# Optimization experiments

Measured on AMD Instinct MI355X. Metric: run time of the kernel, lower is better.

The kernel has to match this reference:

```python
import jax, jax.numpy as jnp
import numpy as np

B = 32768
N_INT = 32          # num_intruders
OWN_D = 3
INT_D = 7
ATTN_D = 128
HID = 256
OUT_D = 2
OBS_D = OWN_D + N_INT * INT_D  # 227
NEG_SLOPE = 0.2

def _lrelu(x):
    return jax.nn.leaky_relu(x, NEG_SLOPE)

def setup_inputs() -> dict:
    key = jax.random.key(0)
    ks = jax.random.split(key, 16)
    obs = jax.random.normal(ks[0], (B, OBS_D), dtype=jnp.float32)
    pad = jax.random.bernoulli(ks[1], 0.25, (B, N_INT))
    intr = obs[:, OWN_D:].reshape(B, N_INT, INT_D)
    intr = jnp.where(pad[:, :, None], 0.0, intr)
    obs = jnp.concatenate([obs[:, :OWN_D], intr.reshape(B, -1)], axis=1)
    def glorot(k, shape):
        fan_in, fan_out = shape[0], shape[-1]
        lim = jnp.sqrt(6.0 / (fan_in + fan_out))
        return jax.random.uniform(k, shape, jnp.float32, -lim, lim)
    return {
        "obs": obs,
        "own_W": glorot(ks[2], (OWN_D, ATTN_D)), "own_b": jnp.zeros((ATTN_D,), jnp.float32),
        "int_W": glorot(ks[3], (INT_D, ATTN_D)), "int_b": jnp.zeros((ATTN_D,), jnp.float32),
        "Wq": glorot(ks[4], (ATTN_D, ATTN_D)),
        "Wk": glorot(ks[5], (ATTN_D, ATTN_D)),
        "Wv": glorot(ks[6], (ATTN_D, ATTN_D)),
        "v_att": glorot(ks[7], (ATTN_D, 1))[:, 0],
        "proj_W": glorot(ks[8], (ATTN_D, ATTN_D)), "proj_b": jnp.zeros((ATTN_D,), jnp.float32),
        "h1_W": glorot(ks[9], (2 * ATTN_D, HID)), "h1_b": jnp.zeros((HID,), jnp.float32),
        "h2_W": glorot(ks[10], (HID, HID)), "h2_b": jnp.zeros((HID,), jnp.float32),
        "out_W": glorot(ks[11], (HID, OUT_D)), "out_b": jnp.zeros((OUT_D,), jnp.float32),
    }

def reference(obs, own_W, own_b, int_W, int_b, Wq, Wk, Wv, v_att,
              proj_W, proj_b, h1_W, h1_b, h2_W, h2_b, out_W, out_b):
    own = obs[:, :OWN_D]                                   # [B,3]
    intr = obs[:, OWN_D:OWN_D + N_INT * INT_D].reshape(-1, N_INT, INT_D)  # [B,N,7]
    own_e = _lrelu(own @ own_W + own_b)                    # [B,128]
    int_e = _lrelu(intr @ int_W + int_b)                   # [B,N,128]
    q = own_e @ Wq                                         # [B,128]
    k = int_e @ Wk                                         # [B,N,128]
    v = int_e @ Wv                                         # [B,N,128]
    energy = jnp.tanh(q[:, None, :] + k)                   # [B,N,128]
    scores = energy @ v_att                                # [B,N]
    is_padding = jnp.abs(intr).sum(axis=2) < 1e-6          # [B,N]
    scores = jnp.where(is_padding, -jnp.inf, scores)
    alpha = jax.nn.softmax(scores, axis=-1)
    alpha = jnp.nan_to_num(alpha, nan=0.0)
    ctx = jnp.einsum('bn,bnd->bd', alpha, v)               # [B,128]
    attn_vec = jnp.tanh(ctx @ proj_W + proj_b)             # [B,128]
    x = jnp.concatenate([own_e, attn_vec], axis=1)         # [B,256]
    x = _lrelu(x @ h1_W + h1_b)
    x = _lrelu(x @ h2_W + h2_b)
    return x @ out_W + out_b                               # [B,2]
```

## Files before the change

kernel.cpp:

```cpp
#include <hip/hip_runtime.h>
#include <hip/hip_bf16.h>
#include <math.h>

typedef _Float16 half2_t __attribute__((ext_vector_type(2)));
typedef _Float16 f16x8   __attribute__((ext_vector_type(8)));
typedef float    f32x4   __attribute__((ext_vector_type(4)));

constexpr int BATCH = 32768;
constexpr int NI   = 32;
constexpr int OWND = 3;
constexpr int INTD = 7;
constexpr int AD   = 128;
constexpr int HIDN = 256;
constexpr int OUTD = 2;
constexpr int OBSD = OWND + NI * INTD;
constexpr int IEPITCH = 68;
constexpr float C2L2E = 2.885390081777927f;

__device__ __forceinline__ half2_t u2h(unsigned u) { return __builtin_bit_cast(half2_t, u); }
__device__ __forceinline__ unsigned packf(float a, float b) {
    half2_t h = { (_Float16)a, (_Float16)b };
    return __builtin_bit_cast(unsigned, h);
}
__device__ __forceinline__ float lrelu(float x) { return fmaxf(x, 0.2f * x); }
__device__ __forceinline__ float exp2fast(float x) { return __builtin_amdgcn_exp2f(x); }
__device__ __forceinline__ float fast_tanh(float x) {
    float e = exp2fast(x * C2L2E);
    return 1.0f - 2.0f * __builtin_amdgcn_rcpf(e + 1.0f);
}

constexpr int UW_PWKQ = 0;
constexpr int UW_PWVF = 16384;
constexpr int UW_PPRF = 24576;
constexpr int UW_PIWF = 32768;
constexpr int UW_PH1F = 34816;
constexpr int UW_PH2F = 67584;
constexpr int UW_FULL = 100352;
constexpr size_t XBUF_U = (size_t)BATCH * (HIDN / 2);

__global__ __launch_bounds__(256) void pack_full(
    const float* __restrict__ Wq, const float* __restrict__ Wk,
    const float* __restrict__ Wv, const float* __restrict__ Pr,
    const float* __restrict__ IW, const float* __restrict__ H1,
    const float* __restrict__ H2, unsigned* __restrict__ dst)
{
    int u = blockIdx.x * 256 + threadIdx.x;
    if (u >= UW_FULL) return;
    if (u < 16384) {
        int f = u >> 8, kt = f >> 3, nt = f & 7;
        int idx = u & 255, lane = idx >> 2, w = idx & 3;
        int qd = lane >> 4, lo = lane & 15;
        const float* src = (kt < 4) ? Wk : Wq;
        int ktp = kt & 3;
        int r0 = 32 * ktp + 8 * qd + 2 * w, col = 16 * nt + lo;
        dst[u] = packf(src[r0 * 128 + col], src[(r0 + 1) * 128 + col]);
    } else if (u < 32768) {
        const float* src = (u < 24576) ? Wv : Pr;
        int i = (u - 16384) & 8191;
        int f = i >> 8, kt = f >> 3, nt = f & 7;
        int idx = i & 255, lane = idx >> 2, w = idx & 3;
        int qd = lane >> 4, lo = lane & 15;
        int r0 = 32 * kt + 8 * qd + 2 * w, col = 16 * nt + lo;
        dst[u] = packf(src[r0 * 128 + col], src[(r0 + 1) * 128 + col]);
    } else if (u < 34816) {
        int i = u - 32768;
        int nt = i >> 8;
        int idx = i & 255, lane = idx >> 2, w = idx & 3;
        int qd = lane >> 4, lo = lane & 15;
        int r0 = 8 * qd + 2 * w, col = 16 * nt + lo;
        float v0 = (r0     < INTD) ? IW[r0 * 128 + col]       : 0.f;
        float v1 = (r0 + 1 < INTD) ? IW[(r0 + 1) * 128 + col] : 0.f;
        dst[u] = packf(v0, v1);
    } else {
        int i = u - 34816;
        const float* src = (i < 32768) ? H1 : H2;
        i &= 32767;
        int f = i >> 8, nt = f >> 3, kt = f & 7;
        int idx = i & 255, lane = idx >> 2, w = idx & 3;
        int qd = lane >> 4, lo = lane & 15;
        int r0 = 32 * kt + 8 * qd + 2 * w, col = 16 * nt + lo;
        dst[u] = packf(src[r0 * 256 + col], src[(r0 + 1) * 256 + col]);
    }
}

__global__ __launch_bounds__(256) void qgemm(
    const float* __restrict__ obs, const float* __restrict__ own_W,
    const float* __restrict__ own_b, const unsigned* __restrict__ pWkqF,
    float* __restrict__ qall)
{
    const int wv = threadIdx.x >> 6;
    const int l  = threadIdx.x & 63;
    const int lo = l & 15, qd = l >> 4;
    const size_t row0 = (size_t)blockIdx.x * 64 + (size_t)wv * 16;

    __shared__ __align__(16) float    s_own[4][16][4];
    __shared__ __align__(16) unsigned s_oe[4][16 * 68];

    if (l < 16) {
        const float* orow = obs + (row0 + l) * OBSD;
        s_own[wv][l][0] = orow[0]; s_own[wv][l][1] = orow[1]; s_own[wv][l][2] = orow[2];
    }

    {
        const float x0 = s_own[wv][lo][0], x1 = s_own[wv][lo][1], x2 = s_own[wv][lo][2];
        #pragma unroll
        for (int jj = 0; jj < 8; jj++) {
            const int c4 = qd * 32 + jj * 4;
            float4 wb = *(const float4*)(own_b + c4);
            float4 w0 = *(const float4*)(own_W + 0 * AD + c4);
            float4 w1 = *(const float4*)(own_W + 1 * AD + c4);
            float4 w2 = *(const float4*)(own_W + 2 * AD + c4);
            float v0 = lrelu(wb.x + x0 * w0.x + x1 * w1.x + x2 * w2.x);
            float v1 = lrelu(wb.y + x0 * w0.y + x1 * w1.y + x2 * w2.y);
            float v2 = lrelu(wb.z + x0 * w0.z + x1 * w1.z + x2 * w2.z);
            float v3 = lrelu(wb.w + x0 * w0.w + x1 * w1.w + x2 * w2.w);
            s_oe[wv][lo * 68 + (c4 >> 1)]     = packf(v0, v1);
            s_oe[wv][lo * 68 + (c4 >> 1) + 1] = packf(v2, v3);
        }
    }

    f16x8 aE[4];
    #pragma unroll
    for (int kt = 0; kt < 4; kt++) {
        uint4 au = *(const uint4*)(&s_oe[wv][lo * 68 + 16 * kt + 4 * qd]);
        aE[kt] = __builtin_bit_cast(f16x8, au);
    }
    #pragma unroll
    for (int nt = 0; nt < 8; nt++) {
        f32x4 acc = {0.f, 0.f, 0.f, 0.f};
        #pragma unroll
        for (int kt = 0; kt < 4; kt++) {
            uint4 bu = *(const uint4*)(pWkqF + (((kt + 4) * 8 + nt) << 8) + (l << 2));
            acc = __builtin_amdgcn_mfma_f32_16x16x32_f16(aE[kt], __builtin_bit_cast(f16x8, bu), acc, 0, 0, 0);
        }
        #pragma unroll
        for (int r = 0; r < 4; r++)
            qall[(row0 + 4 * qd + r) * AD + 16 * nt + lo] = acc[r];
    }
}

__global__ __launch_bounds__(256) void attn(
    const float* __restrict__ obs,
    const float* __restrict__ own_W, const float* __restrict__ own_b,
    const unsigned* __restrict__ pIWF, const float* __restrict__ int_b,
    const unsigned* __restrict__ pWkqF, const float* __restrict__ v_att,
    const float* __restrict__ qall,
    unsigned* __restrict__ xbuf)
{
    const int wv = threadIdx.x >> 6;
    const int l  = threadIdx.x & 63;
    const int b  = blockIdx.x * 4 + wv;
    const int d0 = 2 * l;
    const int lo = l & 15, qd = l >> 4;
    const bool useQ = (qall != nullptr);

    __shared__ __align__(16) float    s_obs[4][OBSD];
    __shared__ __align__(16) unsigned s_ieb[4][NI * IEPITCH];
    __shared__ __align__(16) unsigned s_ownh[4][AD / 2];
    __shared__ __align__(16) float    s_sc[4][NI];

    const float* orow = obs + (size_t)b * OBSD;
    for (int i = l; i < OBSD; i += 64) s_obs[wv][i] = orow[i];

    float oe0 = own_b[d0], oe1 = own_b[d0 + 1];
    #pragma unroll
    for (int j = 0; j < OWND; j++) {
        float x = s_obs[wv][j];
        oe0 += x * own_W[j * AD + d0];
        oe1 += x * own_W[j * AD + d0 + 1];
    }
    oe0 = lrelu(oe0); oe1 = lrelu(oe1);
    s_ownh[wv][l] = packf(oe0, oe1);

    int padf = 0;
    if (l < NI) {
        float su = 0.f;
        #pragma unroll
        for (int j = 0; j < INTD; j++) su += fabsf(s_obs[wv][OWND + l * INTD + j]);
        padf = (su < 1e-6f);
    }

    float qe[8];
    if (useQ) {
        const float* qrow = qall + (size_t)b * AD;
        #pragma unroll
        for (int nt = 0; nt < 8; nt++) qe[nt] = qrow[16 * nt + lo] * C2L2E;
    } else {
        #pragma unroll
        for (int nt = 0; nt < 8; nt++) qe[nt] = 0.f;
    }

    f16x8 aInt[2];
    #pragma unroll
    for (int t = 0; t < 2; t++) {
        #pragma unroll
        for (int j = 0; j < 8; j++) {
            int k = 8 * qd + j;
            float v = (k < INTD) ? s_obs[wv][OWND + (16 * t + lo) * INTD + k] : 0.f;
            aInt[t][j] = (_Float16)v;
        }
    }
    _Float16* s_ieh = (_Float16*)s_ieb[wv];
    #pragma unroll
    for (int nt = 0; nt < 8; nt++) {
        uint4 bu = *(const uint4*)(pIWF + (nt << 8) + (l << 2));
        f16x8 bf = __builtin_bit_cast(f16x8, bu);
        f32x4 z = {0.f, 0.f, 0.f, 0.f};
        f32x4 c0 = __builtin_amdgcn_mfma_f32_16x16x32_f16(aInt[0], bf, z, 0, 0, 0);
        f32x4 c1 = __builtin_amdgcn_mfma_f32_16x16x32_f16(aInt[1], bf, z, 0, 0, 0);
        const float bn = int_b[16 * nt + lo];
        const int cswz = (16 * nt + lo) ^ (qd << 3);
        #pragma unroll
        for (int r = 0; r < 4; r++) {
            s_ieh[(4 * qd + r) * 136 + cswz]      = (_Float16)lrelu(c0[r] + bn);
            s_ieh[(16 + 4 * qd + r) * 136 + cswz] = (_Float16)lrelu(c1[r] + bn);
        }
    }

    const int slo = ((lo >> 2) & 3) << 2;
    f16x8 aIE[2][4];
    #pragma unroll
    for (int t = 0; t < 2; t++)
        #pragma unroll
        for (int kt = 0; kt < 4; kt++) {
            uint4 au = *(const uint4*)(&s_ieb[wv][(16 * t + lo) * IEPITCH + ((16 * kt + 4 * qd) ^ slo)]);
            aIE[t][kt] = __builtin_bit_cast(f16x8, au);
        }

    float sA0[4] = {0.f, 0.f, 0.f, 0.f};
    float sA1[4] = {0.f, 0.f, 0.f, 0.f};
    float vsum = 0.f;
    #pragma unroll
    for (int nt = 0; nt < 8; nt++) {
        f32x4 acc0 = {0.f, 0.f, 0.f, 0.f};
        f32x4 acc1 = {0.f, 0.f, 0.f, 0.f};
        if (useQ) {
            #pragma unroll
            for (int kt = 0; kt < 4; kt++) {
                uint4 bu = *(const uint4*)(pWkqF + ((kt * 8 + nt) << 8) + (l << 2));
                f16x8 bf = __builtin_bit_cast(f16x8, bu);
                acc0 = __builtin_amdgcn_mfma_f32_16x16x32_f16(aIE[0][kt], bf, acc0, 0, 0, 0);
                acc1 = __builtin_amdgcn_mfma_f32_16x16x32_f16(aIE[1][kt], bf, acc1, 0, 0, 0);
            }
        } else {
            #pragma unroll
            for (int kt = 0; kt < 8; kt++) {
                uint4 bu = *(const uint4*)(pWkqF + ((kt * 8 + nt) << 8) + (l << 2));
                f16x8 bf = __builtin_bit_cast(f16x8, bu);
                f16x8 af0, af1;
                if (kt < 4) { af0 = aIE[0][kt]; af1 = aIE[1][kt]; }
                else {
                    uint4 au = *(const uint4*)(&s_ownh[wv][16 * (kt - 4) + 4 * qd]);
                    af0 = __builtin_bit_cast(f16x8, au);
                    af1 = af0;
                }
                acc0 = __builtin_amdgcn_mfma_f32_16x16x32_f16(af0, bf, acc0, 0, 0, 0);
                acc1 = __builtin_amdgcn_mfma_f32_16x16x32_f16(af1, bf, acc1, 0, 0, 0);
            }
        }
        const float vc   = v_att[16 * nt + lo];
        const float n2vc = -2.0f * vc;
        vsum += vc;
        #pragma unroll
        for (int r = 0; r < 4; r++) {
            float t0 = exp2fast(fmaf(acc0[r], C2L2E, qe[nt]));
            sA0[r] = fmaf(n2vc, __builtin_amdgcn_rcpf(t0 + 1.0f), sA0[r]);
            float t1 = exp2fast(fmaf(acc1[r], C2L2E, qe[nt]));
            sA1[r] = fmaf(n2vc, __builtin_amdgcn_rcpf(t1 + 1.0f), sA1[r]);
        }
    }
    #pragma unroll
    for (int r = 0; r < 4; r++) { sA0[r] += vsum; sA1[r] += vsum; }
    #pragma unroll
    for (int r = 0; r < 4; r++) {
        #pragma unroll
        for (int w = 1; w <= 8; w <<= 1) {
            sA0[r] += __shfl_xor(sA0[r], w, 64);
            sA1[r] += __shfl_xor(sA1[r], w, 64);
        }
    }
    if (lo == 0) {
        #pragma unroll
        for (int r = 0; r < 4; r++) {
            s_sc[wv][4 * qd + r]      = sA0[r];
            s_sc[wv][16 + 4 * qd + r] = sA1[r];
        }
    }

    {
        float sval = -INFINITY;
        if (l < NI && !padf) sval = s_sc[wv][l];
        float mm = sval;
        #pragma unroll
        for (int w = 1; w <= 16; w <<= 1) mm = fmaxf(mm, __shfl_xor(mm, w, 64));
        float e = (sval > -INFINITY) ? __expf(sval - mm) : 0.f;
        float dd = e;
        #pragma unroll
        for (int w = 1; w <= 16; w <<= 1) dd += __shfl_xor(dd, w, 64);
        if (l < NI) s_sc[wv][l] = (dd > 0.f) ? e * __builtin_amdgcn_rcpf(dd) : 0.f;
    }

    float sv0 = 0.f, sv1 = 0.f;
    #pragma unroll
    for (int n = 0; n < NI; n++) {
        const int sn = ((n >> 2) & 3) << 2;
        half2_t ie = u2h(s_ieb[wv][n * IEPITCH + (l ^ sn)]);
        float a = s_sc[wv][n];
        sv0 += a * (float)ie.x; sv1 += a * (float)ie.y;
    }
    xbuf[(size_t)b * (HIDN / 2) + l]      = s_ownh[wv][l];
    xbuf[(size_t)b * (HIDN / 2) + 64 + l] = packf(sv0, sv1);
}

__global__ __launch_bounds__(256, 6) void mlp16(
    const unsigned* __restrict__ xbuf,
    const unsigned* __restrict__ pWvF, const float* __restrict__ proj_b,
    const unsigned* __restrict__ pPrF,
    const unsigned* __restrict__ pH1F, const float* __restrict__ h1_b,
    const unsigned* __restrict__ pH2F, const float* __restrict__ h2_b,
    const float* __restrict__ out_W,   const float* __restrict__ out_b,
    float* __restrict__ res)
{
    const int g   = blockIdx.x;
    const int tid = threadIdx.x;
    const int wv  = tid >> 6;
    const int l   = tid & 63;
    const int lo  = l & 15, qd = l >> 4;
    const size_t row0 = (size_t)g * 16;

    __shared__ __align__(16) unsigned s_x[16 * 132];
    __shared__ __align__(16) unsigned s_scr[16 * 68];
    __shared__ __align__(16) float    s_red[4][16][2];

    for (int i = tid; i < 16 * 128; i += 256) {
        int r = i >> 7, c = i & 127;
        unsigned u = xbuf[(row0 + r) * 128 + c];
        if (c < 64) s_x[r * 132 + c] = u;
        else        s_scr[r * 68 + (c - 64)] = u;
    }
    __syncthreads();

    f16x8 aS[4];
    #pragma unroll
    for (int kt = 0; kt < 4; kt++) {
        uint4 au = *(const uint4*)(&s_scr[lo * 68 + 16 * kt + 4 * qd]);
        aS[kt] = __builtin_bit_cast(f16x8, au);
    }
    __syncthreads();
    _Float16* s_ctxh = (_Float16*)s_scr;
    #pragma unroll
    for (int ni = 0; ni < 2; ni++) {
        const int nt = 2 * wv + ni;
        f32x4 acc = {0.f, 0.f, 0.f, 0.f};
        #pragma unroll
        for (int kt = 0; kt < 4; kt++) {
            uint4 bu = *(const uint4*)(pWvF + ((kt * 8 + nt) << 8) + (l << 2));
            acc = __builtin_amdgcn_mfma_f32_16x16x32_f16(aS[kt], __builtin_bit_cast(f16x8, bu), acc, 0, 0, 0);
        }
        #pragma unroll
        for (int r = 0; r < 4; r++)
            s_ctxh[(4 * qd + r) * 136 + 16 * nt + lo] = (_Float16)acc[r];
    }
    __syncthreads();

    f16x8 aC[4];
    #pragma unroll
    for (int kt = 0; kt < 4; kt++) {
        uint4 au = *(const uint4*)(&s_scr[lo * 68 + 16 * kt + 4 * qd]);
        aC[kt] = __builtin_bit_cast(f16x8, au);
    }
    _Float16* s_xh = (_Float16*)s_x;
    #pragma unroll
    for (int ni = 0; ni < 2; ni++) {
        const int nt = 2 * wv + ni;
        f32x4 acc = {0.f, 0.f, 0.f, 0.f};
        #pragma unroll
        for (int kt = 0; kt < 4; kt++) {
            uint4 bu = *(const uint4*)(pPrF + ((kt * 8 + nt) << 8) + (l << 2));
            acc = __builtin_amdgcn_mfma_f32_16x16x32_f16(aC[kt], __builtin_bit_cast(f16x8, bu), acc, 0, 0, 0);
        }
        const float bn = proj_b[16 * nt + lo];
        #pragma unroll
        for (int r = 0; r < 4; r++)
            s_xh[(4 * qd + r) * 264 + 128 + 16 * nt + lo] = (_Float16)fast_tanh(acc[r] + bn);
    }
    __syncthreads();

    f16x8 aX[8];
    #pragma unroll
    for (int kt = 0; kt < 8; kt++) {
        uint4 au = *(const uint4*)(&s_x[lo * 132 + 16 * kt + 4 * qd]);
        aX[kt] = __builtin_bit_cast(f16x8, au);
    }
    __syncthreads();
    #pragma unroll
    for (int ni = 0; ni < 4; ni++) {
        const int nt = 4 * wv + ni;
        f32x4 acc = {0.f, 0.f, 0.f, 0.f};
        #pragma unroll
        for (int kt = 0; kt < 8; kt++) {
            uint4 bu = *(const uint4*)(pH1F + ((nt * 8 + kt) << 8) + (l << 2));
            acc = __builtin_amdgcn_mfma_f32_16x16x32_f16(aX[kt], __builtin_bit_cast(f16x8, bu), acc, 0, 0, 0);
        }
        const float bn = h1_b[16 * nt + lo];
        #pragma unroll
        for (int r = 0; r < 4; r++)
            s_xh[(4 * qd + r) * 264 + 16 * nt + lo] = (_Float16)lrelu(acc[r] + bn);
    }
    __syncthreads();

    f16x8 aH[8];
    #pragma unroll
    for (int kt = 0; kt < 8; kt++) {
        uint4 au = *(const uint4*)(&s_x[lo * 132 + 16 * kt + 4 * qd]);
        aH[kt] = __builtin_bit_cast(f16x8, au);
    }
    float o0[4] = {0.f, 0.f, 0.f, 0.f};
    float o1[4] = {0.f, 0.f, 0.f, 0.f};
    #pragma unroll
    for (int ni = 0; ni < 4; ni++) {
        const int nt = 4 * wv + ni;
        f32x4 acc = {0.f, 0.f, 0.f, 0.f};
        #pragma unroll
        for (int kt = 0; kt < 8; kt++) {
            uint4 bu = *(const uint4*)(pH2F + ((nt * 8 + kt) << 8) + (l << 2));
            acc = __builtin_amdgcn_mfma_f32_16x16x32_f16(aH[kt], __builtin_bit_cast(f16x8, bu), acc, 0, 0, 0);
        }
        const float bn = h2_b[16 * nt + lo];
        float2 w = *(const float2*)(out_W + (size_t)(16 * nt + lo) * OUTD);
        #pragma unroll
        for (int r = 0; r < 4; r++) {
            float v = lrelu(acc[r] + bn);
            o0[r] += v * w.x; o1[r] += v * w.y;
        }
    }
    #pragma unroll
    for (int r = 0; r < 4; r++) {
        #pragma unroll
        for (int w = 1; w <= 8; w <<= 1) {
            o0[r] += __shfl_xor(o0[r], w, 64);
            o1[r] += __shfl_xor(o1[r], w, 64);
        }
    }
    if (lo == 0) {
        #pragma unroll
        for (int r = 0; r < 4; r++) {
            s_red[wv][4 * qd + r][0] = o0[r];
            s_red[wv][4 * qd + r][1] = o1[r];
        }
    }
    __syncthreads();
    if (tid < 32) {
        int r = tid >> 1, cmp = tid & 1;
        float s = s_red[0][r][cmp] + s_red[1][r][cmp]
                + s_red[2][r][cmp] + s_red[3][r][cmp] + out_b[cmp];
        res[(row0 + r) * OUTD + cmp] = s;
    }
}

__global__ __launch_bounds__(256) void copy_out(const float* __restrict__ src,
                                               float* __restrict__ dst, int n4) {
    int i = blockIdx.x * 256 + threadIdx.x;
    if (i < n4) ((float4*)dst)[i] = ((const float4*)src)[i];
}

extern "C" void kernel_launch(void* const* d_in, const int* in_sizes, int n_in,
                              void* d_out, int out_size, void* d_ws, size_t ws_size,
                              hipStream_t stream) {
    const float* obs    = (const float*)d_in[0];
    const float* own_W  = (const float*)d_in[1];
    const float* own_b  = (const float*)d_in[2];
    const float* int_W  = (const float*)d_in[3];
    const float* int_b  = (const float*)d_in[4];
    const float* Wq     = (const float*)d_in[5];
    const float* Wk     = (const float*)d_in[6];
    const float* Wv     = (const float*)d_in[7];
    const float* v_att  = (const float*)d_in[8];
    const float* proj_W = (const float*)d_in[9];
    const float* proj_b = (const float*)d_in[10];
    const float* h1_W   = (const float*)d_in[11];
    const float* h1_b   = (const float*)d_in[12];
    const float* h2_W   = (const float*)d_in[13];
    const float* h2_b   = (const float*)d_in[14];
    const float* out_W  = (const float*)d_in[15];
    const float* out_b  = (const float*)d_in[16];

    const size_t res_bytes  = (size_t)BATCH * OUTD * sizeof(float);
    const size_t q_bytes    = (size_t)BATCH * AD * sizeof(float);
    const size_t base_bytes = (size_t)UW_FULL * 4 + XBUF_U * 4 + res_bytes;
    const int n4 = BATCH * OUTD / 4;

    if (ws_size >= base_bytes + q_bytes) {
        unsigned* pw   = (unsigned*)d_ws;
        unsigned* xbuf = pw + UW_FULL;
        float*    qall = (float*)(xbuf + XBUF_U);
        float*    res  = qall + (size_t)BATCH * AD;
        pack_full<<<(UW_FULL + 255) / 256, 256, 0, stream>>>(
            Wq, Wk, Wv, proj_W, int_W, h1_W, h2_W, pw);
        qgemm<<<BATCH / 64, 256, 0, stream>>>(obs, own_W, own_b, pw + UW_PWKQ, qall);
        attn<<<BATCH / 4, 256, 0, stream>>>(
            obs, own_W, own_b, pw + UW_PIWF, int_b,
            pw + UW_PWKQ, v_att, qall, xbuf);
        mlp16<<<BATCH / 16, 256, 0, stream>>>(
            xbuf, pw + UW_PWVF, proj_b, pw + UW_PPRF,
            pw + UW_PH1F, h1_b, pw + UW_PH2F, h2_b, out_W, out_b, res);
        copy_out<<<(n4 + 255) / 256, 256, 0, stream>>>(res, (float*)d_out, n4);
    } else if (ws_size >= base_bytes) {
        unsigned* pw   = (unsigned*)d_ws;
        unsigned* xbuf = pw + UW_FULL;
        float*    res  = (float*)(xbuf + XBUF_U);
        pack_full<<<(UW_FULL + 255) / 256, 256, 0, stream>>>(
            Wq, Wk, Wv, proj_W, int_W, h1_W, h2_W, pw);
        attn<<<BATCH / 4, 256, 0, stream>>>(
            obs, own_W, own_b, pw + UW_PIWF, int_b,
            pw + UW_PWKQ, v_att, nullptr, xbuf);
        mlp16<<<BATCH / 16, 256, 0, stream>>>(
            xbuf, pw + UW_PWVF, proj_b, pw + UW_PPRF,
            pw + UW_PH1F, h1_b, pw + UW_PH2F, h2_b, out_W, out_b, res);
        copy_out<<<(n4 + 255) / 256, 256, 0, stream>>>(res, (float*)d_out, n4);
    }
}
```

Baseline: 246.6 us.

## Process 32 rows per MLP block to amortize weight fragment loads

The MLP kernel now handles 32 batch rows per block instead of 16, running each GEMM stage twice over two 16-row groups with the same weight tiles. It also switches the xbuf staging load to 16-byte vector loads and drops the occupancy hint in launch bounds. The aim is to halve per-row global and L2 traffic for weight fragments and reduce the number of blocks. The cost is double the shared memory, more sequential work per block, and fewer blocks for latency hiding.

```diff
diff --git a/kernel.cpp b/kernel.cpp
--- a/kernel.cpp
+++ b/kernel.cpp
@@ -312,7 +312,7 @@
     xbuf[(size_t)b * (HIDN / 2) + 64 + l] = packf(sv0, sv1);
 }
 
-__global__ __launch_bounds__(256, 6) void mlp16(
+__global__ __launch_bounds__(256) void mlp32(
     const unsigned* __restrict__ xbuf,
     const unsigned* __restrict__ pWvF, const float* __restrict__ proj_b,
     const unsigned* __restrict__ pPrF,
@@ -321,136 +321,172 @@
     const float* __restrict__ out_W,   const float* __restrict__ out_b,
     float* __restrict__ res)
 {
-    const int g   = blockIdx.x;
     const int tid = threadIdx.x;
     const int wv  = tid >> 6;
     const int l   = tid & 63;
     const int lo  = l & 15, qd = l >> 4;
-    const size_t row0 = (size_t)g * 16;
-
-    __shared__ __align__(16) unsigned s_x[16 * 132];
-    __shared__ __align__(16) unsigned s_scr[16 * 68];
-    __shared__ __align__(16) float    s_red[4][16][2];
-
-    for (int i = tid; i < 16 * 128; i += 256) {
-        int r = i >> 7, c = i & 127;
-        unsigned u = xbuf[(row0 + r) * 128 + c];
-        if (c < 64) s_x[r * 132 + c] = u;
-        else        s_scr[r * 68 + (c - 64)] = u;
+    const size_t row0 = (size_t)blockIdx.x * 32;
+
+    __shared__ __align__(16) unsigned s_x[32 * 132];
+    __shared__ __align__(16) unsigned s_scr[32 * 68];
+    __shared__ __align__(16) float    s_red[4][32][2];
+
+    #pragma unroll
+    for (int it = 0; it < 4; it++) {
+        int i = tid + it * 256;
+        int r = i >> 5, cq = i & 31;
+        uint4 u = *(const uint4*)(xbuf + (row0 + r) * 128 + cq * 4);
+        if (cq < 16) *(uint4*)(&s_x[r * 132 + cq * 4]) = u;
+        else         *(uint4*)(&s_scr[r * 68 + (cq - 16) * 4]) = u;
     }
     __syncthreads();
 
-    f16x8 aS[4];
-    #pragma unroll
-    for (int kt = 0; kt < 4; kt++) {
-        uint4 au = *(const uint4*)(&s_scr[lo * 68 + 16 * kt + 4 * qd]);
-        aS[kt] = __builtin_bit_cast(f16x8, au);
+    _Float16* s_ctxh = (_Float16*)s_scr;
+    _Float16* s_xh   = (_Float16*)s_x;
+
+    #pragma unroll
+    for (int rowg = 0; rowg < 2; rowg++) {
+        const int rb = 16 * rowg;
+        f16x8 aS[4];
+        #pragma unroll
+        for (int kt = 0; kt < 4; kt++) {
+            uint4 au = *(const uint4*)(&s_scr[(rb + lo) * 68 + 16 * kt + 4 * qd]);
+            aS[kt] = __builtin_bit_cast(f16x8, au);
+        }
+        __syncthreads();
+        #pragma unroll
+        for (int ni = 0; ni < 2; ni++) {
+            const int nt = 2 * wv + ni;
+            f32x4 acc = {0.f, 0.f, 0.f, 0.f};
+            #pragma unroll
+            for (int kt = 0; kt < 4; kt++) {
+                uint4 bu = *(const uint4*)(pWvF + ((kt * 8 + nt) << 8) + (l << 2));
+                acc = __builtin_amdgcn_mfma_f32_16x16x32_f16(aS[kt], __builtin_bit_cast(f16x8, bu), acc, 0, 0, 0);
+            }
+            #pragma unroll
+            for (int r = 0; r < 4; r++)
+                s_ctxh[(rb + 4 * qd + r) * 136 + 16 * nt + lo] = (_Float16)acc[r];
+        }
     }
     __syncthreads();
-    _Float16* s_ctxh = (_Float16*)s_scr;
-    #pragma unroll
-    for (int ni = 0; ni < 2; ni++) {
-        const int nt = 2 * wv + ni;
-        f32x4 acc = {0.f, 0.f, 0.f, 0.f};
+
+    #pragma unroll
+    for (int rowg = 0; rowg < 2; rowg++) {
+        const int rb = 16 * rowg;
+        f16x8 aC[4];
         #pragma unroll
         for (int kt = 0; kt < 4; kt++) {
-            uint4 bu = *(const uint4*)(pWvF + ((kt * 8 + nt) << 8) + (l << 2));
-            acc = __builtin_amdgcn_mfma_f32_16x16x32_f16(aS[kt], __builtin_bit_cast(f16x8, bu), acc, 0, 0, 0);
-        }
-        #pragma unroll
-        for (int r = 0; r < 4; r++)
-            s_ctxh[(4 * qd + r) * 136 + 16 * nt + lo] = (_Float16)acc[r];
+            uint4 au = *(const uint4*)(&s_scr[(rb + lo) * 68 + 16 * kt + 4 * qd]);
+            aC[kt] = __builtin_bit_cast(f16x8, au);
+        }
+        #pragma unroll
+        for (int ni = 0; ni < 2; ni++) {
+            const int nt = 2 * wv + ni;
+            f32x4 acc = {0.f, 0.f, 0.f, 0.f};
+            #pragma unroll
+            for (int kt = 0; kt < 4; kt++) {
+                uint4 bu = *(const uint4*)(pPrF + ((kt * 8 + nt) << 8) + (l << 2));
+                acc = __builtin_amdgcn_mfma_f32_16x16x32_f16(aC[kt], __builtin_bit_cast(f16x8, bu), acc, 0, 0, 0);
+            }
+            const float bn = proj_b[16 * nt + lo];
+            #pragma unroll
+            for (int r = 0; r < 4; r++)
+                s_xh[(rb + 4 * qd + r) * 264 + 128 + 16 * nt + lo] = (_Float16)fast_tanh(acc[r] + bn);
+        }
     }
     __syncthreads();
 
-    f16x8 aC[4];
-    #pragma unroll
-    for (int kt = 0; kt < 4; kt++) {
-        uint4 au = *(const uint4*)(&s_scr[lo * 68 + 16 * kt + 4 * qd]);
-        aC[kt] = __builtin_bit_cast(f16x8, au);
-    }
-    _Float16* s_xh = (_Float16*)s_x;
-    #pragma unroll
-    for (int ni = 0; ni < 2; ni++) {
-        const int nt = 2 * wv + ni;
-        f32x4 acc = {0.f, 0.f, 0.f, 0.f};
-        #pragma unroll
-        for (int kt = 0; kt < 4; kt++) {
-            uint4 bu = *(const uint4*)(pPrF + ((kt * 8 + nt) << 8) + (l << 2));
-            acc = __builtin_amdgcn_mfma_f32_16x16x32_f16(aC[kt], __builtin_bit_cast(f16x8, bu), acc, 0, 0, 0);
-        }
-        const float bn = proj_b[16 * nt + lo];
-        #pragma unroll
-        for (int r = 0; r < 4; r++)
-            s_xh[(4 * qd + r) * 264 + 128 + 16 * nt + lo] = (_Float16)fast_tanh(acc[r] + bn);
+    {
+        f16x8 aX[8];
+        #pragma unroll
+        for (int kt = 0; kt < 8; kt++) {
+            uint4 au = *(const uint4*)(&s_x[lo * 132 + 16 * kt + 4 * qd]);
+            aX[kt] = __builtin_bit_cast(f16x8, au);
+        }
+        __syncthreads();
+        #pragma unroll
+        for (int ni = 0; ni < 4; ni++) {
+            const int nt = 4 * wv + ni;
+            f32x4 acc = {0.f, 0.f, 0.f, 0.f};
+            #pragma unroll
+            for (int kt = 0; kt < 8; kt++) {
+                uint4 bu = *(const uint4*)(pH1F + ((nt * 8 + kt) << 8) + (l << 2));
+                acc = __builtin_amdgcn_mfma_f32_16x16x32_f16(aX[kt], __builtin_bit_cast(f16x8, bu), acc, 0, 0, 0);
+            }
+            const float bn = h1_b[16 * nt + lo];
+            #pragma unroll
+            for (int r = 0; r < 4; r++)
+                s_xh[(4 * qd + r) * 264 + 16 * nt + lo] = (_Float16)lrelu(acc[r] + bn);
+        }
+        #pragma unroll
+        for (int kt = 0; kt < 8; kt++) {
+            uint4 au = *(const uint4*)(&s_x[(16 + lo) * 132 + 16 * kt + 4 * qd]);
+            aX[kt] = __builtin_bit_cast(f16x8, au);
+        }
+        __syncthreads();
+        #pragma unroll
+        for (int ni = 0; ni < 4; ni++) {
+            const int nt = 4 * wv + ni;
+            f32x4 acc = {0.f, 0.f, 0.f, 0.f};
+            #pragma unroll
+            for (int kt = 0; kt < 8; kt++) {
+                uint4 bu = *(const uint4*)(pH1F + ((nt * 8 + kt) << 8) + (l << 2));
+                acc = __builtin_amdgcn_mfma_f32_16x16x32_f16(aX[kt], __builtin_bit_cast(f16x8, bu), acc, 0, 0, 0);
+            }
+            const float bn = h1_b[16 * nt + lo];
+            #pragma unroll
+            for (int r = 0; r < 4; r++)
+                s_xh[(16 + 4 * qd + r) * 264 + 16 * nt + lo] = (_Float16)lrelu(acc[r] + bn);
+        }
     }
     __syncthreads();
 
-    f16x8 aX[8];
-    #pragma unroll
-    for (int kt = 0; kt < 8; kt++) {
-        uint4 au = *(const uint4*)(&s_x[lo * 132 + 16 * kt + 4 * qd]);
-        aX[kt] = __builtin_bit_cast(f16x8, au);
+    #pragma unroll
+    for (int rowg = 0; rowg < 2; rowg++) {
+        const int rb = 16 * rowg;
+        f16x8 aH[8];
+        #pragma unroll
+        for (int kt = 0; kt < 8; kt++) {
+            uint4 au = *(const uint4*)(&s_x[(rb + lo) * 132 + 16 * kt + 4 * qd]);
+            aH[kt] = __builtin_bit_cast(f16x8, au);
+        }
+        float o0[4] = {0.f, 0.f, 0.f, 0.f};
+        float o1[4] = {0.f, 0.f, 0.f, 0.f};
+        #pragma unroll
+        for (int ni = 0; ni < 4; ni++) {
+            const int nt = 4 * wv + ni;
+            f32x4 acc = {0.f, 0.f, 0.f, 0.f};
+            #pragma unroll
+            for (int kt = 0; kt < 8; kt++) {
+                uint4 bu = *(const uint4*)(pH2F + ((nt * 8 + kt) << 8) + (l << 2));
+                acc = __builtin_amdgcn_mfma_f32_16x16x32_f16(aH[kt], __builtin_bit_cast(f16x8, bu), acc, 0, 0, 0);
+            }
+            const float bn = h2_b[16 * nt + lo];
+            float2 w = *(const float2*)(out_W + (size_t)(16 * nt + lo) * OUTD);
+            #pragma unroll
+            for (int r = 0; r < 4; r++) {
+                float v = lrelu(acc[r] + bn);
+                o0[r] += v * w.x; o1[r] += v * w.y;
+            }
+        }
+        #pragma unroll
+        for (int r = 0; r < 4; r++) {
+            #pragma unroll
+            for (int w = 1; w <= 8; w <<= 1) {
+                o0[r] += __shfl_xor(o0[r], w, 64);
+                o1[r] += __shfl_xor(o1[r], w, 64);
+            }
+        }
+        if (lo == 0) {
+            #pragma unroll
+            for (int r = 0; r < 4; r++) {
+                s_red[wv][rb + 4 * qd + r][0] = o0[r];
+                s_red[wv][rb + 4 * qd + r][1] = o1[r];
+            }
+        }
     }
     __syncthreads();
-    #pragma unroll
-    for (int ni = 0; ni < 4; ni++) {
-        const int nt = 4 * wv + ni;
-        f32x4 acc = {0.f, 0.f, 0.f, 0.f};
-        #pragma unroll
-        for (int kt = 0; kt < 8; kt++) {
-            uint4 bu = *(const uint4*)(pH1F + ((nt * 8 + kt) << 8) + (l << 2));
-            acc = __builtin_amdgcn_mfma_f32_16x16x32_f16(aX[kt], __builtin_bit_cast(f16x8, bu), acc, 0, 0, 0);
-        }
-        const float bn = h1_b[16 * nt + lo];
-        #pragma unroll
-        for (int r = 0; r < 4; r++)
-            s_xh[(4 * qd + r) * 264 + 16 * nt + lo] = (_Float16)lrelu(acc[r] + bn);
-    }
-    __syncthreads();
-
-    f16x8 aH[8];
-    #pragma unroll
-    for (int kt = 0; kt < 8; kt++) {
-        uint4 au = *(const uint4*)(&s_x[lo * 132 + 16 * kt + 4 * qd]);
-        aH[kt] = __builtin_bit_cast(f16x8, au);
-    }
-    float o0[4] = {0.f, 0.f, 0.f, 0.f};
-    float o1[4] = {0.f, 0.f, 0.f, 0.f};
-    #pragma unroll
-    for (int ni = 0; ni < 4; ni++) {
-        const int nt = 4 * wv + ni;
-        f32x4 acc = {0.f, 0.f, 0.f, 0.f};
-        #pragma unroll
-        for (int kt = 0; kt < 8; kt++) {
-            uint4 bu = *(const uint4*)(pH2F + ((nt * 8 + kt) << 8) + (l << 2));
-            acc = __builtin_amdgcn_mfma_f32_16x16x32_f16(aH[kt], __builtin_bit_cast(f16x8, bu), acc, 0, 0, 0);
-        }
-        const float bn = h2_b[16 * nt + lo];
-        float2 w = *(const float2*)(out_W + (size_t)(16 * nt + lo) * OUTD);
-        #pragma unroll
-        for (int r = 0; r < 4; r++) {
-            float v = lrelu(acc[r] + bn);
-            o0[r] += v * w.x; o1[r] += v * w.y;
-        }
-    }
-    #pragma unroll
-    for (int r = 0; r < 4; r++) {
-        #pragma unroll
-        for (int w = 1; w <= 8; w <<= 1) {
-            o0[r] += __shfl_xor(o0[r], w, 64);
-            o1[r] += __shfl_xor(o1[r], w, 64);
-        }
-    }
-    if (lo == 0) {
-        #pragma unroll
-        for (int r = 0; r < 4; r++) {
-            s_red[wv][4 * qd + r][0] = o0[r];
-            s_red[wv][4 * qd + r][1] = o1[r];
-        }
-    }
-    __syncthreads();
-    if (tid < 32) {
+    if (tid < 64) {
         int r = tid >> 1, cmp = tid & 1;
         float s = s_red[0][r][cmp] + s_red[1][r][cmp]
                 + s_red[2][r][cmp] + s_red[3][r][cmp] + out_b[cmp];
@@ -501,7 +537,7 @@
         attn<<<BATCH / 4, 256, 0, stream>>>(
             obs, own_W, own_b, pw + UW_PIWF, int_b,
             pw + UW_PWKQ, v_att, qall, xbuf);
-        mlp16<<<BATCH / 16, 256, 0, stream>>>(
+        mlp32<<<BATCH / 32, 256, 0, stream>>>(
             xbuf, pw + UW_PWVF, proj_b, pw + UW_PPRF,
             pw + UW_PH1F, h1_b, pw + UW_PH2F, h2_b, out_W, out_b, res);
         copy_out<<<(n4 + 255) / 256, 256, 0, stream>>>(res, (float*)d_out, n4);
@@ -514,7 +550,7 @@
         attn<<<BATCH / 4, 256, 0, stream>>>(
             obs, own_W, own_b, pw + UW_PIWF, int_b,
             pw + UW_PWKQ, v_att, nullptr, xbuf);
-        mlp16<<<BATCH / 16, 256, 0, stream>>>(
+        mlp32<<<BATCH / 32, 256, 0, stream>>>(
             xbuf, pw + UW_PWVF, proj_b, pw + UW_PPRF,
             pw + UW_PH1F, h1_b, pw + UW_PH2F, h2_b, out_W, out_b, res);
         copy_out<<<(n4 + 255) / 256, 256, 0, stream>>>(res, (float*)d_out, n4);
```

New measurement: 243.4 us. No clear change (-1.3%).
